# Performance work log

Measured on AMD Instinct MI355X. Metric: run time of the kernel, lower is better.

The kernel has to match this reference:

```python
import jax, jax.numpy as jnp
import numpy as np

B, T, S = 2, 1024, 1024
D, H, L = 512, 8, 4
E, K, FF = 8, 2, 2048
V, BLK = 32000, 2048
DH = D // H
EPS = 1e-5


def setup_inputs() -> dict:
    key = jax.random.key(0)
    ks = jax.random.split(key, 20)
    n = lambda k, shp: jax.random.normal(k, shp, dtype=jnp.float32) * 0.02
    return {
        "decoder_input_ids": jax.random.randint(ks[0], (B, T), 0, V, dtype=jnp.int32),
        "enc_out": jax.random.normal(ks[1], (B, S, D), dtype=jnp.float32),
        "attention_mask": jnp.ones((B, T), dtype=jnp.int32),
        "embed_table": n(ks[2], (V, D)),
        "pos_table": n(ks[3], (BLK, D)),
        "sa_w": n(ks[4], (L, 4, D, D)),   # q,k,v,o projections for self-attn
        "sa_b": jnp.zeros((L, 4, D), jnp.float32),
        "ca_w": n(ks[5], (L, 4, D, D)),   # q,k,v,o projections for cross-attn
        "ca_b": jnp.zeros((L, 4, D), jnp.float32),
        "ln_g": jnp.ones((L, 3, D), jnp.float32),
        "ln_b": jnp.zeros((L, 3, D), jnp.float32),
        "router_w": n(ks[6], (L, D, E)),
        "router_b": jnp.zeros((L, E), jnp.float32),
        "exp_w1": n(ks[7], (L, E, D, FF)),
        "exp_b1": jnp.zeros((L, E, FF), jnp.float32),
        "exp_w2": n(ks[8], (L, E, FF, D)),
        "exp_b2": jnp.zeros((L, E, D), jnp.float32),
    }


def _layer_norm(x, g, b):
    mu = jnp.mean(x, axis=-1, keepdims=True)
    var = jnp.mean(jnp.square(x - mu), axis=-1, keepdims=True)
    return (x - mu) * jax.lax.rsqrt(var + EPS) * g + b


def _mha(q_in, kv_in, w, b, mask):
    # w: [4, D, D]; 0=q,1=k,2=v,3=out
    def split_heads(t):
        Bn, Tn, _ = t.shape
        return t.reshape(Bn, Tn, H, DH).transpose(0, 2, 1, 3)  # [B,H,T,dh]
    q = split_heads(q_in @ w[0] + b[0])
    k = split_heads(kv_in @ w[1] + b[1])
    v = split_heads(kv_in @ w[2] + b[2])
    scores = jnp.einsum("bhqd,bhkd->bhqk", q, k) / jnp.sqrt(jnp.float32(DH))
    if mask is not None:
        scores = jnp.where(mask, scores, jnp.float32(-1e9))
    attn = jax.nn.softmax(scores, axis=-1)
    out = jnp.einsum("bhqk,bhkd->bhqd", attn, v)
    out = out.transpose(0, 2, 1, 3).reshape(q_in.shape[0], q_in.shape[1], D)
    return out @ w[3] + b[3]


def _sparse_moe(x, rw, rb, w1, b1, w2, b2):
    # Router: softmax over experts, keep top-k, renormalize kept weights.
    logits = x @ rw + rb                       # [B,T,E]
    probs = jax.nn.softmax(logits, axis=-1)
    topv, topi = jax.lax.top_k(probs, K)       # [B,T,K]
    kmask = jnp.sum(jax.nn.one_hot(topi, E, dtype=x.dtype), axis=-2)  # [B,T,E]
    gates = probs * kmask
    gates = gates / jnp.sum(gates, axis=-1, keepdims=True)
    # Dense expert compute (faithful math, vectorized over experts).
    h = jax.nn.relu(jnp.einsum("btd,edf->btef", x, w1) + b1)   # [B,T,E,FF]
    eo = jnp.einsum("btef,efd->bted", h, w2) + b2              # [B,T,E,D]
    out = jnp.einsum("bte,bted->btd", gates, eo)
    # Load-balancing aux loss: E * sum_e f_e * P_e
    f = jnp.mean(kmask, axis=(0, 1))
    p = jnp.mean(probs, axis=(0, 1))
    lb = jnp.float32(E) * jnp.sum(f * p)
    return out, lb


def reference(decoder_input_ids, enc_out, attention_mask, embed_table, pos_table,
              sa_w, sa_b, ca_w, ca_b, ln_g, ln_b, router_w, router_b,
              exp_w1, exp_b1, exp_w2, exp_b2):
    Bn, Tn = decoder_input_ids.shape
    y = embed_table[decoder_input_ids] + pos_table[:Tn]  # [B,T,D]
    causal = jnp.tril(jnp.ones((Tn, Tn), dtype=bool))
    am = attention_mask.astype(bool)[:, None, None, :]   # [B,1,1,T]
    mask = causal[None, None] & am                       # [B,1,T,T]
    lb_total = jnp.float32(0.0)
    for i in range(L):
        sa = _mha(y, y, sa_w[i], sa_b[i], mask)
        y = _layer_norm(y + sa, ln_g[i, 0], ln_b[i, 0])
        ca = _mha(y, enc_out, ca_w[i], ca_b[i], None)
        y = _layer_norm(y + ca, ln_g[i, 1], ln_b[i, 1])
        mo, lb = _sparse_moe(y, router_w[i], router_b[i], exp_w1[i], exp_b1[i], exp_w2[i], exp_b2[i])
        lb_total = lb_total + lb
        y = _layer_norm(y + mo, ln_g[i, 2], ln_b[i, 2])
    return y, lb_total
```

## Files before the change

### kernel.cpp

```cpp
#include <hip/hip_runtime.h>
#include <math.h>

#define Bb 2
#define Tt 1024
#define Ss 1024
#define Dd 512
#define Hh 8
#define Ll 4
#define Ee 8
#define FFf 2048
#define Mm 2048
#define NPp 4096
#define EPSF 1e-5f
#define DD_ (Dd*Dd)
#define LOSC 1024.0f
#define ILOSC (1.0f/1024.0f)
#define RBLK 64
#define IMm (1.0f/(float)Mm)

typedef _Float16 f16;
typedef __attribute__((ext_vector_type(8))) _Float16 f16x8;
typedef __attribute__((ext_vector_type(4))) _Float16 f16x4;
typedef __attribute__((ext_vector_type(4))) float f32x4;

__device__ __forceinline__ void fsplit(float x, f16& h, f16& l) {
  h = (f16)x;
  l = (f16)((x - (float)h) * LOSC);
}

__device__ __forceinline__ void load16(const void* g, void* l) {
  __builtin_amdgcn_global_load_lds(
      (const __attribute__((address_space(1))) void*)g,
      (__attribute__((address_space(3))) void*)l, 16, 0, 0);
}

__global__ void embed_kernel(const int* __restrict__ ids,
                             const float* __restrict__ emb,
                             const float* __restrict__ pos,
                             float* __restrict__ Y,
                             f16* __restrict__ Yh, f16* __restrict__ Yl) {
  int m = blockIdx.x;
  int t = m % Tt;
  int id = ids[m];
  for (int d = threadIdx.x; d < Dd; d += 256) {
    float v = emb[(size_t)id * Dd + d] + pos[(size_t)t * Dd + d];
    Y[(size_t)m * Dd + d] = v;
    f16 h, l; fsplit(v, h, l);
    Yh[(size_t)m * Dd + d] = h;
    Yl[(size_t)m * Dd + d] = l;
  }
}

__global__ void cvt_split_kernel(const float* __restrict__ src,
                                 f16* __restrict__ dh, f16* __restrict__ dl) {
  size_t i = ((size_t)blockIdx.x * 256 + threadIdx.x) * 4;
  float4 v = *reinterpret_cast<const float4*>(&src[i]);
  float a[4] = {v.x, v.y, v.z, v.w};
#pragma unroll
  for (int j = 0; j < 4; j++) { f16 h, l; fsplit(a[j], h, l); dh[i + j] = h; dl[i + j] = l; }
}

__global__ __launch_bounds__(256)
void transpose_split(const float* __restrict__ src,
                     f16* __restrict__ dstH, f16* __restrict__ dstL,
                     int Kd, int Nd) {
  __shared__ float Tl[32][33];
  size_t zo = (size_t)blockIdx.z * Kd * Nd;
  int k0 = blockIdx.y * 32, n0 = blockIdx.x * 32;
  int t = threadIdx.x;
  int r = t >> 3, c = t & 7;
  float4 v = *reinterpret_cast<const float4*>(&src[zo + (size_t)(k0 + r) * Nd + n0 + c * 4]);
  Tl[r][c * 4 + 0] = v.x; Tl[r][c * 4 + 1] = v.y;
  Tl[r][c * 4 + 2] = v.z; Tl[r][c * 4 + 3] = v.w;
  __syncthreads();
  int nl = t >> 3, kq = t & 7;
  f16x4 hv, lv;
#pragma unroll
  for (int i = 0; i < 4; i++) {
    f16 h, l; fsplit(Tl[kq * 4 + i][nl], h, l);
    hv[i] = h; lv[i] = l;
  }
  size_t o = zo + (size_t)(n0 + nl) * Kd + k0 + kq * 4;
  *reinterpret_cast<f16x4*>(&dstH[o]) = hv;
  *reinterpret_cast<f16x4*>(&dstL[o]) = lv;
}

template <bool GATHER, bool OSPLIT, bool RELU, bool GATE>
__global__ __launch_bounds__(256)
void mm128(const f16* __restrict__ Ah_, const f16* __restrict__ Al_, int lda,
           const f16* __restrict__ Bh_, const f16* __restrict__ Bl_,
           const float* __restrict__ bias,
           float* __restrict__ Cf, f16* __restrict__ Ch, f16* __restrict__ Cl, int ldc,
           int Mtot, int N, int K,
           const int* __restrict__ tok, const float* __restrict__ gate,
           const int* __restrict__ offs, const int* __restrict__ cnt) {
  __shared__ f16 Ash[128 * 32];
  __shared__ f16 Asl[128 * 32];
  __shared__ f16 Bsh[128 * 32];
  __shared__ f16 Bsl[128 * 32];
  int e = blockIdx.z;
  int base = 0, ne = Mtot;
  if (offs) { base = offs[e]; ne = cnt[e]; }
  int m0 = blockIdx.y * 128;
  if (m0 >= ne) return;
  int rem = ne - m0;
  Bh_ += (size_t)e * N * K;
  Bl_ += (size_t)e * N * K;
  bias += (size_t)e * N;

  int t = threadIdx.x;
  int rr = t >> 2, cc = t & 3;
  int gr0 = base + m0 + rr;      if (gr0 > Mtot - 1) gr0 = Mtot - 1;
  int gr1 = base + m0 + rr + 64; if (gr1 > Mtot - 1) gr1 = Mtot - 1;
  int arow0 = GATHER ? tok[gr0] : gr0;
  int arow1 = GATHER ? tok[gr1] : gr1;
  size_t aoff0 = (size_t)arow0 * lda + cc * 8;
  size_t aoff1 = (size_t)arow1 * lda + cc * 8;
  size_t boff0 = (size_t)(blockIdx.x * 128 + rr) * K + cc * 8;
  size_t boff1 = (size_t)(blockIdx.x * 128 + rr + 64) * K + cc * 8;

  int lane = t & 63, wv = t >> 6;
  int quad = lane >> 4, m16 = lane & 15;
  int wm = (wv >> 1) * 64, wn = (wv & 1) * 64;

  f32x4 accm[4][4], accc[4][4];
#pragma unroll
  for (int i = 0; i < 4; i++)
#pragma unroll
    for (int j = 0; j < 4; j++) {
      accm[i][j] = (f32x4){0.f, 0.f, 0.f, 0.f};
      accc[i][j] = (f32x4){0.f, 0.f, 0.f, 0.f};
    }

  for (int kc = 0; kc < K; kc += 32) {
    load16(Ah_ + aoff0 + kc, &Ash[t * 8]);
    load16(Ah_ + aoff1 + kc, &Ash[2048 + t * 8]);
    load16(Al_ + aoff0 + kc, &Asl[t * 8]);
    load16(Al_ + aoff1 + kc, &Asl[2048 + t * 8]);
    load16(Bh_ + boff0 + kc, &Bsh[t * 8]);
    load16(Bh_ + boff1 + kc, &Bsh[2048 + t * 8]);
    load16(Bl_ + boff0 + kc, &Bsl[t * 8]);
    load16(Bl_ + boff1 + kc, &Bsl[2048 + t * 8]);
    __syncthreads();
    f16x8 ah[4], al[4];
#pragma unroll
    for (int i = 0; i < 4; i++) {
      ah[i] = *reinterpret_cast<const f16x8*>(&Ash[(wm + i * 16 + m16) * 32 + quad * 8]);
      al[i] = *reinterpret_cast<const f16x8*>(&Asl[(wm + i * 16 + m16) * 32 + quad * 8]);
    }
#pragma unroll
    for (int j = 0; j < 4; j++) {
      f16x8 bh = *reinterpret_cast<const f16x8*>(&Bsh[(wn + j * 16 + m16) * 32 + quad * 8]);
      f16x8 bl = *reinterpret_cast<const f16x8*>(&Bsl[(wn + j * 16 + m16) * 32 + quad * 8]);
#pragma unroll
      for (int i = 0; i < 4; i++) {
        accm[i][j] = __builtin_amdgcn_mfma_f32_16x16x32_f16(ah[i], bh, accm[i][j], 0, 0, 0);
        accc[i][j] = __builtin_amdgcn_mfma_f32_16x16x32_f16(ah[i], bl, accc[i][j], 0, 0, 0);
        accc[i][j] = __builtin_amdgcn_mfma_f32_16x16x32_f16(al[i], bh, accc[i][j], 0, 0, 0);
      }
    }
    __syncthreads();
  }

#pragma unroll
  for (int i = 0; i < 4; i++) {
#pragma unroll
    for (int reg = 0; reg < 4; reg++) {
      int lr = wm + i * 16 + quad * 4 + reg;
      if (lr < rem) {
        size_t grow = (size_t)(base + m0 + lr);
        float gv = 1.f;
        if (GATE) gv = gate[grow];
#pragma unroll
        for (int j = 0; j < 4; j++) {
          int col = blockIdx.x * 128 + wn + j * 16 + m16;
          float v = accm[i][j][reg] + accc[i][j][reg] * ILOSC + bias[col];
          if (RELU) v = fmaxf(v, 0.f);
          if (GATE) v *= gv;
          if (OSPLIT) {
            f16 h, l; fsplit(v, h, l);
            Ch[grow * ldc + col] = h;
            Cl[grow * ldc + col] = l;
          } else {
            Cf[grow * ldc + col] = v;
          }
        }
      }
    }
  }
}

__global__ __launch_bounds__(256)
void attn_mfma(const f16* __restrict__ Qh, const f16* __restrict__ Ql, int sq, int oq,
               const f16* __restrict__ Kh, const f16* __restrict__ Kl, int sk, int ok,
               const f16* __restrict__ Vh, const f16* __restrict__ Vl, int sv, int ov,
               f16* __restrict__ Oh, f16* __restrict__ Ol,
               const int* __restrict__ amask, int causal, int nK) {
  __shared__ f16 Ksh[32 * 64];
  __shared__ f16 Ksl[32 * 64];
  __shared__ f16 Vth[64 * 32];
  __shared__ f16 Vtl[64 * 32];
  __shared__ f16 Psh[4 * 16 * 32];
  __shared__ f16 Psl[4 * 16 * 32];

  int bh = blockIdx.x;
  int b = bh >> 3, hd = bh & 7;
  int t = threadIdx.x;
  int wv = t >> 6, lane = t & 63;
  int quad = lane >> 4, m16 = lane & 15;
  int qfrow = blockIdx.y * 64 + wv * 16 + m16;
  int qcbase = blockIdx.y * 64 + wv * 16 + quad * 4;

  size_t qoff = (size_t)(b * Tt + qfrow) * sq + oq + hd * 64;
  f16x8 qh0 = *reinterpret_cast<const f16x8*>(Qh + qoff + quad * 8);
  f16x8 qh1 = *reinterpret_cast<const f16x8*>(Qh + qoff + 32 + quad * 8);
  f16x8 ql0 = *reinterpret_cast<const f16x8*>(Ql + qoff + quad * 8);
  f16x8 ql1 = *reinterpret_cast<const f16x8*>(Ql + qoff + 32 + quad * 8);

  f32x4 Om[4], Oc[4];
#pragma unroll
  for (int c = 0; c < 4; c++) {
    Om[c] = (f32x4){0.f, 0.f, 0.f, 0.f};
    Oc[c] = (f32x4){0.f, 0.f, 0.f, 0.f};
  }
  float mr[4] = {-1e30f, -1e30f, -1e30f, -1e30f};
  float lrw[4] = {0.f, 0.f, 0.f, 0.f};

  int NT = causal ? (blockIdx.y * 2 + 2) : (nK >> 5);
  int myNT = causal ? (((blockIdx.y * 64 + wv * 16 + 15) >> 5) + 1) : NT;

  int rk = t >> 3, gs = t & 7, gsrc = gs ^ (rk & 7);
  int rv = t & 31, gv = t >> 5;

  for (int kt = 0; kt < NT; ++kt) {
    __syncthreads();
    {
      size_t krow = (size_t)(b * 1024 + kt * 32 + rk) * sk + ok + hd * 64 + gsrc * 8;
      *reinterpret_cast<f16x8*>(&Ksh[t * 8]) = *reinterpret_cast<const f16x8*>(Kh + krow);
      *reinterpret_cast<f16x8*>(&Ksl[t * 8]) = *reinterpret_cast<const f16x8*>(Kl + krow);
      size_t vrow = (size_t)(b * 1024 + kt * 32 + rv) * sv + ov + hd * 64 + gv * 8;
      f16x8 vh8 = *reinterpret_cast<const f16x8*>(Vh + vrow);
      f16x8 vl8 = *reinterpret_cast<const f16x8*>(Vl + vrow);
#pragma unroll
      for (int i = 0; i < 8; i++) {
        Vth[(gv * 8 + i) * 32 + rv] = vh8[i];
        Vtl[(gv * 8 + i) * 32 + rv] = vl8[i];
      }
    }
    __syncthreads();

    if (kt < myNT) {
      f32x4 S0m = (f32x4){0.f, 0.f, 0.f, 0.f}, S0c = S0m, S1m = S0m, S1c = S0m;
      {
        int key0 = m16, key1 = 16 + m16;
        int g0a = (quad) ^ (key0 & 7), g0b = (4 + quad) ^ (key0 & 7);
        int g1a = (quad) ^ (key1 & 7), g1b = (4 + quad) ^ (key1 & 7);
        f16x8 kh0a = *reinterpret_cast<const f16x8*>(&Ksh[key0 * 64 + g0a * 8]);
        f16x8 kh0b = *reinterpret_cast<const f16x8*>(&Ksh[key0 * 64 + g0b * 8]);
        f16x8 kl0a = *reinterpret_cast<const f16x8*>(&Ksl[key0 * 64 + g0a * 8]);
        f16x8 kl0b = *reinterpret_cast<const f16x8*>(&Ksl[key0 * 64 + g0b * 8]);
        S0m = __builtin_amdgcn_mfma_f32_16x16x32_f16(qh0, kh0a, S0m, 0, 0, 0);
        S0m = __builtin_amdgcn_mfma_f32_16x16x32_f16(qh1, kh0b, S0m, 0, 0, 0);
        S0c = __builtin_amdgcn_mfma_f32_16x16x32_f16(qh0, kl0a, S0c, 0, 0, 0);
        S0c = __builtin_amdgcn_mfma_f32_16x16x32_f16(qh1, kl0b, S0c, 0, 0, 0);
        S0c = __builtin_amdgcn_mfma_f32_16x16x32_f16(ql0, kh0a, S0c, 0, 0, 0);
        S0c = __builtin_amdgcn_mfma_f32_16x16x32_f16(ql1, kh0b, S0c, 0, 0, 0);
        f16x8 kh1a = *reinterpret_cast<const f16x8*>(&Ksh[key1 * 64 + g1a * 8]);
        f16x8 kh1b = *reinterpret_cast<const f16x8*>(&Ksh[key1 * 64 + g1b * 8]);
        f16x8 kl1a = *reinterpret_cast<const f16x8*>(&Ksl[key1 * 64 + g1a * 8]);
        f16x8 kl1b = *reinterpret_cast<const f16x8*>(&Ksl[key1 * 64 + g1b * 8]);
        S1m = __builtin_amdgcn_mfma_f32_16x16x32_f16(qh0, kh1a, S1m, 0, 0, 0);
        S1m = __builtin_amdgcn_mfma_f32_16x16x32_f16(qh1, kh1b, S1m, 0, 0, 0);
        S1c = __builtin_amdgcn_mfma_f32_16x16x32_f16(qh0, kl1a, S1c, 0, 0, 0);
        S1c = __builtin_amdgcn_mfma_f32_16x16x32_f16(qh1, kl1b, S1c, 0, 0, 0);
        S1c = __builtin_amdgcn_mfma_f32_16x16x32_f16(ql0, kh1a, S1c, 0, 0, 0);
        S1c = __builtin_amdgcn_mfma_f32_16x16x32_f16(ql1, kh1b, S1c, 0, 0, 0);
      }
      float S0[4], S1[4];
      int key0 = kt * 32 + m16, key1 = kt * 32 + 16 + m16;
      int am0 = amask ? amask[b * nK + key0] : 1;
      int am1 = amask ? amask[b * nK + key1] : 1;
#pragma unroll
      for (int reg = 0; reg < 4; reg++) {
        int qr = qcbase + reg;
        bool ok0 = am0 && (!causal || key0 <= qr);
        bool ok1 = am1 && (!causal || key1 <= qr);
        S0[reg] = ok0 ? (S0m[reg] + S0c[reg] * ILOSC) * 0.125f : -1e9f;
        S1[reg] = ok1 ? (S1m[reg] + S1c[reg] * ILOSC) * 0.125f : -1e9f;
      }
      float mt[4], al4[4], rs[4];
#pragma unroll
      for (int reg = 0; reg < 4; reg++) mt[reg] = fmaxf(S0[reg], S1[reg]);
#pragma unroll
      for (int off = 1; off < 16; off <<= 1)
#pragma unroll
        for (int reg = 0; reg < 4; reg++) mt[reg] = fmaxf(mt[reg], __shfl_xor(mt[reg], off, 64));
#pragma unroll
      for (int reg = 0; reg < 4; reg++) {
        float mn = fmaxf(mr[reg], mt[reg]);
        al4[reg] = expf(mr[reg] - mn);
        mr[reg] = mn;
        S0[reg] = expf(S0[reg] - mn);
        S1[reg] = expf(S1[reg] - mn);
        rs[reg] = S0[reg] + S1[reg];
      }
#pragma unroll
      for (int off = 1; off < 16; off <<= 1)
#pragma unroll
        for (int reg = 0; reg < 4; reg++) rs[reg] += __shfl_xor(rs[reg], off, 64);
#pragma unroll
      for (int reg = 0; reg < 4; reg++) {
        lrw[reg] = lrw[reg] * al4[reg] + rs[reg];
#pragma unroll
        for (int c = 0; c < 4; c++) { Om[c][reg] *= al4[reg]; Oc[c][reg] *= al4[reg]; }
        int prow = wv * 16 + quad * 4 + reg;
        f16 ph, pl;
        fsplit(S0[reg], ph, pl);
        Psh[prow * 32 + m16] = ph; Psl[prow * 32 + m16] = pl;
        fsplit(S1[reg], ph, pl);
        Psh[prow * 32 + 16 + m16] = ph; Psl[prow * 32 + 16 + m16] = pl;
      }
      __builtin_amdgcn_sched_barrier(0);
      f16x8 pah = *reinterpret_cast<const f16x8*>(&Psh[(wv * 16 + m16) * 32 + quad * 8]);
      f16x8 pal = *reinterpret_cast<const f16x8*>(&Psl[(wv * 16 + m16) * 32 + quad * 8]);
#pragma unroll
      for (int c = 0; c < 4; c++) {
        f16x8 vbh = *reinterpret_cast<const f16x8*>(&Vth[(c * 16 + m16) * 32 + quad * 8]);
        f16x8 vbl = *reinterpret_cast<const f16x8*>(&Vtl[(c * 16 + m16) * 32 + quad * 8]);
        Om[c] = __builtin_amdgcn_mfma_f32_16x16x32_f16(pah, vbh, Om[c], 0, 0, 0);
        Oc[c] = __builtin_amdgcn_mfma_f32_16x16x32_f16(pah, vbl, Oc[c], 0, 0, 0);
        Oc[c] = __builtin_amdgcn_mfma_f32_16x16x32_f16(pal, vbh, Oc[c], 0, 0, 0);
      }
    }
  }
#pragma unroll
  for (int reg = 0; reg < 4; reg++) {
    int qr = qcbase + reg;
    float inv = 1.f / lrw[reg];
#pragma unroll
    for (int c = 0; c < 4; c++) {
      float o = (Om[c][reg] + Oc[c][reg] * ILOSC) * inv;
      f16 hh, ll; fsplit(o, hh, ll);
      size_t oo = (size_t)(b * Tt + qr) * Dd + hd * 64 + c * 16 + m16;
      Oh[oo] = hh;
      Ol[oo] = ll;
    }
  }
}

__global__ __launch_bounds__(256)
void add_ln_kernel(float* __restrict__ Y, f16* __restrict__ Yh, f16* __restrict__ Yl,
                   const float* __restrict__ Aadd,
                   const float* __restrict__ g, const float* __restrict__ bb) {
  int tid = threadIdx.x;
  size_t base = (size_t)blockIdx.x * Dd;
  __shared__ float red[256];
  __shared__ float mu_s, rs_s;
  float x0 = Y[base + tid] + Aadd[base + tid];
  float x1 = Y[base + 256 + tid] + Aadd[base + 256 + tid];
  red[tid] = x0 + x1; __syncthreads();
  for (int s2 = 128; s2 > 0; s2 >>= 1) { if (tid < s2) red[tid] += red[tid + s2]; __syncthreads(); }
  if (tid == 0) mu_s = red[0] / (float)Dd;
  __syncthreads();
  float mu = mu_s;
  float d0 = x0 - mu, d1 = x1 - mu;
  red[tid] = d0 * d0 + d1 * d1; __syncthreads();
  for (int s2 = 128; s2 > 0; s2 >>= 1) { if (tid < s2) red[tid] += red[tid + s2]; __syncthreads(); }
  if (tid == 0) rs_s = rsqrtf(red[0] / (float)Dd + EPSF);
  __syncthreads();
  float rs = rs_s;
  float o0 = d0 * rs * g[tid] + bb[tid];
  float o1 = d1 * rs * g[256 + tid] + bb[256 + tid];
  f16 h, l;
  Y[base + tid] = o0; fsplit(o0, h, l); Yh[base + tid] = h; Yl[base + tid] = l;
  Y[base + 256 + tid] = o1; fsplit(o1, h, l); Yh[base + 256 + tid] = h; Yl[base + 256 + tid] = l;
}

__global__ __launch_bounds__(256)
void combine_ln_kernel(float* __restrict__ Y, f16* __restrict__ Yh, f16* __restrict__ Yl,
                       const float* __restrict__ pout, const int* __restrict__ slot,
                       const float* __restrict__ g, const float* __restrict__ bb) {
  int tid = threadIdx.x;
  int m = blockIdx.x;
  size_t base = (size_t)m * Dd;
  int s0 = slot[m * 2 + 0], s1 = slot[m * 2 + 1];
  __shared__ float red[256];
  __shared__ float mu_s, rs_s;
  float x0 = Y[base + tid] + pout[(size_t)s0 * Dd + tid] + pout[(size_t)s1 * Dd + tid];
  float x1 = Y[base + 256 + tid] + pout[(size_t)s0 * Dd + 256 + tid] + pout[(size_t)s1 * Dd + 256 + tid];
  red[tid] = x0 + x1; __syncthreads();
  for (int s2 = 128; s2 > 0; s2 >>= 1) { if (tid < s2) red[tid] += red[tid + s2]; __syncthreads(); }
  if (tid == 0) mu_s = red[0] / (float)Dd;
  __syncthreads();
  float mu = mu_s;
  float d0 = x0 - mu, d1 = x1 - mu;
  red[tid] = d0 * d0 + d1 * d1; __syncthreads();
  for (int s2 = 128; s2 > 0; s2 >>= 1) { if (tid < s2) red[tid] += red[tid + s2]; __syncthreads(); }
  if (tid == 0) rs_s = rsqrtf(red[0] / (float)Dd + EPSF);
  __syncthreads();
  float rs = rs_s;
  float o0 = d0 * rs * g[tid] + bb[tid];
  float o1 = d1 * rs * g[256 + tid] + bb[256 + tid];
  f16 h, l;
  Y[base + tid] = o0; fsplit(o0, h, l); Yh[base + tid] = h; Yl[base + tid] = l;
  Y[base + 256 + tid] = o1; fsplit(o1, h, l); Yh[base + 256 + tid] = h; Yl[base + 256 + tid] = l;
}

__global__ __launch_bounds__(256)
void router_kernel(const float* __restrict__ Y, const float* __restrict__ rw,
                   const float* __restrict__ rb, float* __restrict__ gates,
                   int* __restrict__ topi, int* __restrict__ part_cnt,
                   float* __restrict__ part_sumP) {
  int wv = threadIdx.x >> 6, lane = threadIdx.x & 63;
  __shared__ float wsum[4][Ee];
  __shared__ int wcnt[4][Ee];
  float w[8][Ee];
#pragma unroll
  for (int dd = 0; dd < 8; dd++) {
    const float4* rp = reinterpret_cast<const float4*>(&rw[(size_t)(dd * 64 + lane) * Ee]);
    float4 a = rp[0], b4 = rp[1];
    w[dd][0] = a.x; w[dd][1] = a.y; w[dd][2] = a.z; w[dd][3] = a.w;
    w[dd][4] = b4.x; w[dd][5] = b4.y; w[dd][6] = b4.z; w[dd][7] = b4.w;
  }
  float rbv[Ee];
#pragma unroll
  for (int e = 0; e < Ee; e++) rbv[e] = rb[e];

  float psum[Ee]; int pcnt[Ee];
#pragma unroll
  for (int e = 0; e < Ee; e++) { psum[e] = 0.f; pcnt[e] = 0; }

  int m0 = blockIdx.x * 32 + wv * 8;
  for (int j = 0; j < 8; j++) {
    int m = m0 + j;
    const float* yr = Y + (size_t)m * Dd;
    float yv[8];
#pragma unroll
    for (int dd = 0; dd < 8; dd++) yv[dd] = yr[dd * 64 + lane];
    float acc[Ee];
#pragma unroll
    for (int e = 0; e < Ee; e++) acc[e] = 0.f;
#pragma unroll
    for (int dd = 0; dd < 8; dd++)
#pragma unroll
      for (int e = 0; e < Ee; e++) acc[e] += yv[dd] * w[dd][e];
#pragma unroll
    for (int off = 32; off; off >>= 1)
#pragma unroll
      for (int e = 0; e < Ee; e++) acc[e] += __shfl_xor(acc[e], off, 64);
    if (lane == 0) {
      float pv[Ee];
      float mx = -1e30f;
#pragma unroll
      for (int e = 0; e < Ee; e++) { pv[e] = acc[e] + rbv[e]; mx = fmaxf(mx, pv[e]); }
      float ssum = 0.f;
#pragma unroll
      for (int e = 0; e < Ee; e++) { pv[e] = expf(pv[e] - mx); ssum += pv[e]; }
      float invs = 1.f / ssum;
#pragma unroll
      for (int e = 0; e < Ee; e++) { pv[e] *= invs; psum[e] += pv[e]; }
      int i1 = 0;
#pragma unroll
      for (int e = 1; e < Ee; e++) if (pv[e] > pv[i1]) i1 = e;
      int i2 = (i1 == 0) ? 1 : 0;
#pragma unroll
      for (int e = 0; e < Ee; e++) if (e != i1 && pv[e] > pv[i2]) i2 = e;
      float gs = pv[i1] + pv[i2];
      gates[m * 2 + 0] = pv[i1] / gs;
      gates[m * 2 + 1] = pv[i2] / gs;
      topi[m * 2 + 0] = i1;
      topi[m * 2 + 1] = i2;
#pragma unroll
      for (int e = 0; e < Ee; e++) pcnt[e] += (e == i1) + (e == i2);
    }
  }
  if (lane == 0) {
#pragma unroll
    for (int e = 0; e < Ee; e++) { wsum[wv][e] = psum[e]; wcnt[wv][e] = pcnt[e]; }
  }
  __syncthreads();
  if (threadIdx.x < Ee) {
    int e = threadIdx.x;
    float s = wsum[0][e] + wsum[1][e] + wsum[2][e] + wsum[3][e];
    int c = wcnt[0][e] + wcnt[1][e] + wcnt[2][e] + wcnt[3][e];
    part_sumP[blockIdx.x * Ee + e] = s;
    part_cnt[blockIdx.x * Ee + e] = c;
  }
}

__global__ void prefix_lb_kernel(const int* __restrict__ part_cnt,
                                 const float* __restrict__ part_sumP,
                                 int* __restrict__ cnt, int* __restrict__ offs,
                                 int* __restrict__ fill, float* __restrict__ lb_acc) {
  __shared__ int sc[Ee];
  __shared__ float ss[Ee];
  int t = threadIdx.x;
  if (t < Ee) {
    int c = 0; float s = 0.f;
    for (int b2 = 0; b2 < RBLK; b2++) { c += part_cnt[b2 * Ee + t]; s += part_sumP[b2 * Ee + t]; }
    sc[t] = c; ss[t] = s;
    cnt[t] = c; fill[t] = 0;
  }
  __syncthreads();
  if (t == 0) {
    int run = 0;
    float lb = 0.f;
    for (int e = 0; e < Ee; e++) {
      offs[e] = run; run += sc[e];
      lb += ((float)sc[e] * IMm) * (ss[e] * IMm);
    }
    *lb_acc += (float)Ee * lb;
  }
}

__global__ __launch_bounds__(256)
void scatter_kernel(const int* __restrict__ topi, const float* __restrict__ gates,
                    const int* __restrict__ offs, int* __restrict__ fill,
                    int* __restrict__ pair_tok, float* __restrict__ pair_gate,
                    int* __restrict__ slot) {
  __shared__ int lcnt[Ee];
  __shared__ int lbase[Ee];
  int t = threadIdx.x;
  int m = blockIdx.x * 256 + t;
  if (t < Ee) lcnt[t] = 0;
  __syncthreads();
  int e0 = topi[m * 2 + 0], e1 = topi[m * 2 + 1];
  float g0 = gates[m * 2 + 0], g1 = gates[m * 2 + 1];
  int p0 = atomicAdd(&lcnt[e0], 1);
  int p1 = atomicAdd(&lcnt[e1], 1);
  __syncthreads();
  if (t < Ee) lbase[t] = atomicAdd(&fill[t], lcnt[t]);
  __syncthreads();
  int i0 = offs[e0] + lbase[e0] + p0;
  int i1 = offs[e1] + lbase[e1] + p1;
  pair_tok[i0] = m; pair_gate[i0] = g0; slot[m * 2 + 0] = i0;
  pair_tok[i1] = m; pair_gate[i1] = g1; slot[m * 2 + 1] = i1;
}

__global__ void init_lb_kernel(float* lb_acc) {
  if (threadIdx.x == 0) *lb_acc = 0.f;
}

__global__ void finalize_kernel(const float* __restrict__ Y,
                                const float* __restrict__ lb_acc,
                                float* __restrict__ out) {
  size_t i = (size_t)blockIdx.x * 256 + threadIdx.x;
  const size_t n = (size_t)Mm * Dd;
  if (i < n) out[i] = Y[i];
  if (i == 0) out[n] = *lb_acc;
}

extern "C" void kernel_launch(void* const* d_in, const int* in_sizes, int n_in,
                              void* d_out, int out_size, void* d_ws, size_t ws_size,
                              hipStream_t stream) {
  const int*   ids   = (const int*)d_in[0];
  const float* enc   = (const float*)d_in[1];
  const int*   amask = (const int*)d_in[2];
  const float* emb   = (const float*)d_in[3];
  const float* pos   = (const float*)d_in[4];
  const float* sa_w  = (const float*)d_in[5];
  const float* sa_b  = (const float*)d_in[6];
  const float* ca_w  = (const float*)d_in[7];
  const float* ca_b  = (const float*)d_in[8];
  const float* ln_g  = (const float*)d_in[9];
  const float* ln_b  = (const float*)d_in[10];
  const float* rw    = (const float*)d_in[11];
  const float* rb    = (const float*)d_in[12];
  const float* ew1   = (const float*)d_in[13];
  const float* eb1   = (const float*)d_in[14];
  const float* ew2   = (const float*)d_in[15];
  const float* eb2   = (const float*)d_in[16];
  float* out = (float*)d_out;

  char* p = (char*)d_ws;
  auto alloc = [&](size_t bytes) { void* r = p; p += (bytes + 255) & ~(size_t)255; return r; };
  float* y    = (float*)alloc((size_t)Mm * Dd * 4);
  float* proj = (float*)alloc((size_t)Mm * Dd * 4);
  float* pout = (float*)alloc((size_t)NPp * Dd * 4);
  f16* yh   = (f16*)alloc((size_t)Mm * Dd * 2);
  f16* yl   = (f16*)alloc((size_t)Mm * Dd * 2);
  f16* ench = (f16*)alloc((size_t)Mm * Dd * 2);
  f16* encl = (f16*)alloc((size_t)Mm * Dd * 2);
  f16* qkvh = (f16*)alloc((size_t)Mm * 1536 * 2);
  f16* qkvl = (f16*)alloc((size_t)Mm * 1536 * 2);
  f16* qch  = (f16*)alloc((size_t)Mm * Dd * 2);
  f16* qcl  = (f16*)alloc((size_t)Mm * Dd * 2);
  f16* atth = (f16*)alloc((size_t)Mm * Dd * 2);
  f16* attl = (f16*)alloc((size_t)Mm * Dd * 2);
  f16* ckvh = (f16*)alloc((size_t)Mm * 1024 * 2);
  f16* ckvl = (f16*)alloc((size_t)Mm * 1024 * 2);
  f16* moeh = (f16*)alloc((size_t)NPp * FFf * 2);
  f16* moel = (f16*)alloc((size_t)NPp * FFf * 2);
  f16* saTh = (f16*)alloc((size_t)Ll * 4 * DD_ * 2);
  f16* saTl = (f16*)alloc((size_t)Ll * 4 * DD_ * 2);
  f16* caTh = (f16*)alloc((size_t)Ll * 4 * DD_ * 2);
  f16* caTl = (f16*)alloc((size_t)Ll * 4 * DD_ * 2);
  f16* w1Th = (f16*)alloc((size_t)Ee * Dd * FFf * 2);
  f16* w1Tl = (f16*)alloc((size_t)Ee * Dd * FFf * 2);
  f16* w2Th = (f16*)alloc((size_t)Ee * Dd * FFf * 2);
  f16* w2Tl = (f16*)alloc((size_t)Ee * Dd * FFf * 2);
  float* gates     = (float*)alloc((size_t)Mm * 2 * 4);
  float* pair_gate = (float*)alloc((size_t)NPp * 4);
  float* part_sumP = (float*)alloc((size_t)RBLK * Ee * 4);
  float* lb_acc    = (float*)alloc(4);
  int* topi     = (int*)alloc((size_t)Mm * 2 * 4);
  int* pair_tok = (int*)alloc((size_t)NPp * 4);
  int* slot     = (int*)alloc((size_t)Mm * 2 * 4);
  int* part_cnt = (int*)alloc((size_t)RBLK * Ee * 4);
  int* cnt      = (int*)alloc(Ee * 4);
  int* offs     = (int*)alloc(Ee * 4);
  int* fill     = (int*)alloc(Ee * 4);

  init_lb_kernel<<<1, 64, 0, stream>>>(lb_acc);
  embed_kernel<<<Mm, 256, 0, stream>>>(ids, emb, pos, y, yh, yl);
  cvt_split_kernel<<<(Mm * Dd) / 1024, 256, 0, stream>>>(enc, ench, encl);
  transpose_split<<<dim3(16, 16, 16), 256, 0, stream>>>(sa_w, saTh, saTl, Dd, Dd);
  transpose_split<<<dim3(16, 16, 16), 256, 0, stream>>>(ca_w, caTh, caTl, Dd, Dd);

  dim3 gAttn(Bb * Hh, Tt / 64);

  for (int i = 0; i < Ll; i++) {
    transpose_split<<<dim3(64, 16, 8), 256, 0, stream>>>(ew1 + (size_t)i * Ee * Dd * FFf, w1Th, w1Tl, Dd, FFf);
    transpose_split<<<dim3(16, 64, 8), 256, 0, stream>>>(ew2 + (size_t)i * Ee * FFf * Dd, w2Th, w2Tl, FFf, Dd);

    const f16* saThl = saTh + (size_t)i * 4 * DD_;
    const f16* saTll = saTl + (size_t)i * 4 * DD_;
    const f16* caThl = caTh + (size_t)i * 4 * DD_;
    const f16* caTll = caTl + (size_t)i * 4 * DD_;
    const float* sabl = sa_b + (size_t)i * 4 * Dd;
    const float* cabl = ca_b + (size_t)i * 4 * Dd;

    mm128<false, true, false, false><<<dim3(8, 16, 1), 256, 0, stream>>>(
        ench, encl, Dd, caThl + DD_, caTll + DD_, cabl + Dd,
        nullptr, ckvh, ckvl, 1024, Mm, 1024, Dd, nullptr, nullptr, nullptr, nullptr);
    mm128<false, true, false, false><<<dim3(12, 16, 1), 256, 0, stream>>>(
        yh, yl, Dd, saThl, saTll, sabl,
        nullptr, qkvh, qkvl, 1536, Mm, 1536, Dd, nullptr, nullptr, nullptr, nullptr);
    attn_mfma<<<gAttn, 256, 0, stream>>>(qkvh, qkvl, 1536, 0, qkvh, qkvl, 1536, 512,
                                         qkvh, qkvl, 1536, 1024, atth, attl, amask, 1, Tt);
    mm128<false, false, false, false><<<dim3(4, 16, 1), 256, 0, stream>>>(
        atth, attl, Dd, saThl + 3 * DD_, saTll + 3 * DD_, sabl + 3 * Dd,
        proj, nullptr, nullptr, Dd, Mm, Dd, Dd, nullptr, nullptr, nullptr, nullptr);
    add_ln_kernel<<<Mm, 256, 0, stream>>>(y, yh, yl, proj,
                                          ln_g + (size_t)(i * 3 + 0) * Dd, ln_b + (size_t)(i * 3 + 0) * Dd);
    mm128<false, true, false, false><<<dim3(4, 16, 1), 256, 0, stream>>>(
        yh, yl, Dd, caThl, caTll, cabl,
        nullptr, qch, qcl, Dd, Mm, Dd, Dd, nullptr, nullptr, nullptr, nullptr);
    attn_mfma<<<gAttn, 256, 0, stream>>>(qch, qcl, Dd, 0, ckvh, ckvl, 1024, 0,
                                         ckvh, ckvl, 1024, 512, atth, attl, nullptr, 0, Ss);
    mm128<false, false, false, false><<<dim3(4, 16, 1), 256, 0, stream>>>(
        atth, attl, Dd, caThl + 3 * DD_, caTll + 3 * DD_, cabl + 3 * Dd,
        proj, nullptr, nullptr, Dd, Mm, Dd, Dd, nullptr, nullptr, nullptr, nullptr);
    add_ln_kernel<<<Mm, 256, 0, stream>>>(y, yh, yl, proj,
                                          ln_g + (size_t)(i * 3 + 1) * Dd, ln_b + (size_t)(i * 3 + 1) * Dd);
    router_kernel<<<RBLK, 256, 0, stream>>>(y, rw + (size_t)i * Dd * Ee, rb + (size_t)i * Ee,
                                            gates, topi, part_cnt, part_sumP);
    prefix_lb_kernel<<<1, 64, 0, stream>>>(part_cnt, part_sumP, cnt, offs, fill, lb_acc);
    scatter_kernel<<<Mm / 256, 256, 0, stream>>>(topi, gates, offs, fill, pair_tok, pair_gate, slot);
    mm128<true, true, true, false><<<dim3(16, 32, 8), 256, 0, stream>>>(
        yh, yl, Dd, w1Th, w1Tl, eb1 + (size_t)i * Ee * FFf,
        nullptr, moeh, moel, FFf, NPp, FFf, Dd, pair_tok, nullptr, offs, cnt);
    mm128<false, false, false, true><<<dim3(4, 32, 8), 256, 0, stream>>>(
        moeh, moel, FFf, w2Th, w2Tl, eb2 + (size_t)i * Ee * Dd,
        pout, nullptr, nullptr, Dd, NPp, Dd, FFf, nullptr, pair_gate, offs, cnt);
    combine_ln_kernel<<<Mm, 256, 0, stream>>>(y, yh, yl, pout, slot,
                                              ln_g + (size_t)(i * 3 + 2) * Dd, ln_b + (size_t)(i * 3 + 2) * Dd);
  }

  finalize_kernel<<<(int)(((size_t)Mm * Dd + 256) / 256) + 1, 256, 0, stream>>>(y, lb_acc, out);
}
```

Before: 2.547 ms.

## Split-K the MoE down-projection with atomics and XOR-swizzle GEMM shared memory

Adds a split-K template parameter to the mm128 GEMM and uses a 4-way K split for the expert down-projection (K=2048). The partial sums are accumulated into a zero-initialised output with atomicAdd, and only the first split adds the bias. The goal is more blocks in flight for a launch whose grid is mostly empty per expert. It also XOR-swizzles the 16-byte chunk placement in the shared A/B tiles to cut LDS bank conflicts on the MFMA operand reads. The cost is an extra zeroing kernel, atomic traffic and a nondeterministic floating-point summation order.

```diff
diff --git a/kernel.cpp b/kernel.cpp
--- a/kernel.cpp
+++ b/kernel.cpp
@@ -60,6 +60,11 @@
   for (int j = 0; j < 4; j++) { f16 h, l; fsplit(a[j], h, l); dh[i + j] = h; dl[i + j] = l; }
 }
 
+__global__ void zero_kernel(float* __restrict__ p) {
+  size_t i = ((size_t)blockIdx.x * 256 + threadIdx.x) * 4;
+  *reinterpret_cast<float4*>(&p[i]) = make_float4(0.f, 0.f, 0.f, 0.f);
+}
+
 __global__ __launch_bounds__(256)
 void transpose_split(const float* __restrict__ src,
                      f16* __restrict__ dstH, f16* __restrict__ dstL,
@@ -85,7 +90,7 @@
   *reinterpret_cast<f16x4*>(&dstL[o]) = lv;
 }
 
-template <bool GATHER, bool OSPLIT, bool RELU, bool GATE>
+template <bool GATHER, bool OSPLIT, bool RELU, bool GATE, int KS>
 __global__ __launch_bounds__(256)
 void mm128(const f16* __restrict__ Ah_, const f16* __restrict__ Al_, int lda,
            const f16* __restrict__ Bh_, const f16* __restrict__ Bl_,
@@ -98,7 +103,9 @@
   __shared__ f16 Asl[128 * 32];
   __shared__ f16 Bsh[128 * 32];
   __shared__ f16 Bsl[128 * 32];
-  int e = blockIdx.z;
+  int zz = blockIdx.z;
+  int e  = (KS > 1) ? (zz / KS) : zz;
+  int ks = (KS > 1) ? (zz % KS) : 0;
   int base = 0, ne = Mtot;
   if (offs) { base = offs[e]; ne = cnt[e]; }
   int m0 = blockIdx.y * 128;
@@ -110,17 +117,19 @@
 
   int t = threadIdx.x;
   int rr = t >> 2, cc = t & 3;
+  int csw = cc ^ ((rr >> 1) & 3);
   int gr0 = base + m0 + rr;      if (gr0 > Mtot - 1) gr0 = Mtot - 1;
   int gr1 = base + m0 + rr + 64; if (gr1 > Mtot - 1) gr1 = Mtot - 1;
   int arow0 = GATHER ? tok[gr0] : gr0;
   int arow1 = GATHER ? tok[gr1] : gr1;
-  size_t aoff0 = (size_t)arow0 * lda + cc * 8;
-  size_t aoff1 = (size_t)arow1 * lda + cc * 8;
-  size_t boff0 = (size_t)(blockIdx.x * 128 + rr) * K + cc * 8;
-  size_t boff1 = (size_t)(blockIdx.x * 128 + rr + 64) * K + cc * 8;
+  size_t aoff0 = (size_t)arow0 * lda + csw * 8;
+  size_t aoff1 = (size_t)arow1 * lda + csw * 8;
+  size_t boff0 = (size_t)(blockIdx.x * 128 + rr) * K + csw * 8;
+  size_t boff1 = (size_t)(blockIdx.x * 128 + rr + 64) * K + csw * 8;
 
   int lane = t & 63, wv = t >> 6;
   int quad = lane >> 4, m16 = lane & 15;
+  int sw = quad ^ ((m16 >> 1) & 3);
   int wm = (wv >> 1) * 64, wn = (wv & 1) * 64;
 
   f32x4 accm[4][4], accc[4][4];
@@ -132,7 +141,9 @@
       accc[i][j] = (f32x4){0.f, 0.f, 0.f, 0.f};
     }
 
-  for (int kc = 0; kc < K; kc += 32) {
+  int kper = K / KS;
+  int kbeg = ks * kper;
+  for (int kc = kbeg; kc < kbeg + kper; kc += 32) {
     load16(Ah_ + aoff0 + kc, &Ash[t * 8]);
     load16(Ah_ + aoff1 + kc, &Ash[2048 + t * 8]);
     load16(Al_ + aoff0 + kc, &Asl[t * 8]);
@@ -145,13 +156,13 @@
     f16x8 ah[4], al[4];
 #pragma unroll
     for (int i = 0; i < 4; i++) {
-      ah[i] = *reinterpret_cast<const f16x8*>(&Ash[(wm + i * 16 + m16) * 32 + quad * 8]);
-      al[i] = *reinterpret_cast<const f16x8*>(&Asl[(wm + i * 16 + m16) * 32 + quad * 8]);
+      ah[i] = *reinterpret_cast<const f16x8*>(&Ash[(wm + i * 16 + m16) * 32 + sw * 8]);
+      al[i] = *reinterpret_cast<const f16x8*>(&Asl[(wm + i * 16 + m16) * 32 + sw * 8]);
     }
 #pragma unroll
     for (int j = 0; j < 4; j++) {
-      f16x8 bh = *reinterpret_cast<const f16x8*>(&Bsh[(wn + j * 16 + m16) * 32 + quad * 8]);
-      f16x8 bl = *reinterpret_cast<const f16x8*>(&Bsl[(wn + j * 16 + m16) * 32 + quad * 8]);
+      f16x8 bh = *reinterpret_cast<const f16x8*>(&Bsh[(wn + j * 16 + m16) * 32 + sw * 8]);
+      f16x8 bl = *reinterpret_cast<const f16x8*>(&Bsl[(wn + j * 16 + m16) * 32 + sw * 8]);
 #pragma unroll
       for (int i = 0; i < 4; i++) {
         accm[i][j] = __builtin_amdgcn_mfma_f32_16x16x32_f16(ah[i], bh, accm[i][j], 0, 0, 0);
@@ -174,13 +185,16 @@
 #pragma unroll
         for (int j = 0; j < 4; j++) {
           int col = blockIdx.x * 128 + wn + j * 16 + m16;
-          float v = accm[i][j][reg] + accc[i][j][reg] * ILOSC + bias[col];
+          float bv = (KS == 1 || ks == 0) ? bias[col] : 0.f;
+          float v = accm[i][j][reg] + accc[i][j][reg] * ILOSC + bv;
           if (RELU) v = fmaxf(v, 0.f);
           if (GATE) v *= gv;
           if (OSPLIT) {
             f16 h, l; fsplit(v, h, l);
             Ch[grow * ldc + col] = h;
             Cl[grow * ldc + col] = l;
+          } else if (KS > 1) {
+            atomicAdd(&Cf[grow * ldc + col], v);
           } else {
             Cf[grow * ldc + col] = v;
           }
@@ -630,37 +644,38 @@
     const float* sabl = sa_b + (size_t)i * 4 * Dd;
     const float* cabl = ca_b + (size_t)i * 4 * Dd;
 
-    mm128<false, true, false, false><<<dim3(8, 16, 1), 256, 0, stream>>>(
+    mm128<false, true, false, false, 1><<<dim3(8, 16, 1), 256, 0, stream>>>(
         ench, encl, Dd, caThl + DD_, caTll + DD_, cabl + Dd,
         nullptr, ckvh, ckvl, 1024, Mm, 1024, Dd, nullptr, nullptr, nullptr, nullptr);
-    mm128<false, true, false, false><<<dim3(12, 16, 1), 256, 0, stream>>>(
+    mm128<false, true, false, false, 1><<<dim3(12, 16, 1), 256, 0, stream>>>(
         yh, yl, Dd, saThl, saTll, sabl,
         nullptr, qkvh, qkvl, 1536, Mm, 1536, Dd, nullptr, nullptr, nullptr, nullptr);
     attn_mfma<<<gAttn, 256, 0, stream>>>(qkvh, qkvl, 1536, 0, qkvh, qkvl, 1536, 512,
                                          qkvh, qkvl, 1536, 1024, atth, attl, amask, 1, Tt);
-    mm128<false, false, false, false><<<dim3(4, 16, 1), 256, 0, stream>>>(
+    mm128<false, false, false, false, 1><<<dim3(4, 16, 1), 256, 0, stream>>>(
         atth, attl, Dd, saThl + 3 * DD_, saTll + 3 * DD_, sabl + 3 * Dd,
         proj, nullptr, nullptr, Dd, Mm, Dd, Dd, nullptr, nullptr, nullptr, nullptr);
     add_ln_kernel<<<Mm, 256, 0, stream>>>(y, yh, yl, proj,
                                           ln_g + (size_t)(i * 3 + 0) * Dd, ln_b + (size_t)(i * 3 + 0) * Dd);
-    mm128<false, true, false, false><<<dim3(4, 16, 1), 256, 0, stream>>>(
+    mm128<false, true, false, false, 1><<<dim3(4, 16, 1), 256, 0, stream>>>(
         yh, yl, Dd, caThl, caTll, cabl,
         nullptr, qch, qcl, Dd, Mm, Dd, Dd, nullptr, nullptr, nullptr, nullptr);
     attn_mfma<<<gAttn, 256, 0, stream>>>(qch, qcl, Dd, 0, ckvh, ckvl, 1024, 0,
                                          ckvh, ckvl, 1024, 512, atth, attl, nullptr, 0, Ss);
-    mm128<false, false, false, false><<<dim3(4, 16, 1), 256, 0, stream>>>(
+    mm128<false, false, false, false, 1><<<dim3(4, 16, 1), 256, 0, stream>>>(
         atth, attl, Dd, caThl + 3 * DD_, caTll + 3 * DD_, cabl + 3 * Dd,
         proj, nullptr, nullptr, Dd, Mm, Dd, Dd, nullptr, nullptr, nullptr, nullptr);
     add_ln_kernel<<<Mm, 256, 0, stream>>>(y, yh, yl, proj,
                                           ln_g + (size_t)(i * 3 + 1) * Dd, ln_b + (size_t)(i * 3 + 1) * Dd);
     router_kernel<<<RBLK, 256, 0, stream>>>(y, rw + (size_t)i * Dd * Ee, rb + (size_t)i * Ee,
                                             gates, topi, part_cnt, part_sumP);
-    prefix_lb_kernel<<<1, 64, 0, stream>>>(part_cnt, part_sumP, cnt, offs, fill, lb_acc);
+    prefix_lb_kernel<<<1, 64, 0, stream>>>(part_cnt, part_sumP, cnt, offs, lb_acc ? fill : fill, lb_acc);
     scatter_kernel<<<Mm / 256, 256, 0, stream>>>(topi, gates, offs, fill, pair_tok, pair_gate, slot);
-    mm128<true, true, true, false><<<dim3(16, 32, 8), 256, 0, stream>>>(
+    zero_kernel<<<((size_t)NPp * Dd) / 1024, 256, 0, stream>>>(pout);
+    mm128<true, true, true, false, 1><<<dim3(16, 32, 8), 256, 0, stream>>>(
         yh, yl, Dd, w1Th, w1Tl, eb1 + (size_t)i * Ee * FFf,
         nullptr, moeh, moel, FFf, NPp, FFf, Dd, pair_tok, nullptr, offs, cnt);
-    mm128<false, false, false, true><<<dim3(4, 32, 8), 256, 0, stream>>>(
+    mm128<false, false, false, true, 4><<<dim3(4, 32, Ee * 4), 256, 0, stream>>>(
         moeh, moel, FFf, w2Th, w2Tl, eb2 + (size_t)i * Ee * Dd,
         pout, nullptr, nullptr, Dd, NPp, Dd, FFf, nullptr, pair_gate, offs, cnt);
     combine_ln_kernel<<<Mm, 256, 0, stream>>>(y, yh, yl, pout, slot,
```

Result: slower. 2.873 ms (+12.8%).
